# Performance work log

Hardware: AMD Instinct MI355X
Metric: run time of the kernel (lower is better)

Reference implementation:

```python
import jax, jax.numpy as jnp
import numpy as np

B, T, N, C = 8, 16, 2048, 512


def setup_inputs() -> dict:
    key = jax.random.key(0)
    k1, k2, k3, k4, k5, k6 = jax.random.split(key, 6)
    return {
        "vd_s": jax.random.normal(k1, (B, T, C), dtype=jnp.float32),
        "vd_nodes": jax.random.normal(k2, (B, N, C), dtype=jnp.float32),
        # 1x1 conv weights initialized N(0, 0.01) as in the torch module
        "W1": jax.random.normal(k3, (C, C), dtype=jnp.float32) * 0.01,
        "b1": jax.random.normal(k4, (C,), dtype=jnp.float32) * 0.01,
        "W2": jax.random.normal(k5, (C, C), dtype=jnp.float32) * 0.01,
        "b2": jax.random.normal(k6, (C,), dtype=jnp.float32) * 0.01,
    }


def reference(vd_s, vd_nodes, W1, b1, W2, b2):
    # propagation_step = 1 (as in the original module)
    def per_graph(s, nodes):
        # s: [T, C] scene features, nodes: [N, C] node features
        out_scene = s.mean(axis=0)                     # [C]
        state = nodes                                  # [N, C]
        # 1x1 convs on [N, C, 1, 1] == per-node linear layers
        mat1 = state @ W1.T + b1                       # [N, C]
        mat2 = state @ W2.T + b2                       # [N, C]
        adj = mat1 @ mat2.T                            # [N, N]
        soft_adj = jax.nn.softmax(adj, axis=1)         # row-softmax (dim=1)
        new_state = soft_adj @ state + state           # message update + residual
        gp_out = new_state.mean(axis=0)                # [C]
        return jnp.concatenate([out_scene, gp_out], axis=0)  # [2C]

    return jax.vmap(per_graph)(vd_s, vd_nodes)         # [B, 2C]
```

## Files before the change

### kernel.cpp

```cpp
#include <hip/hip_runtime.h>

typedef __bf16 bf16;
typedef __bf16 bf16x8 __attribute__((ext_vector_type(8), aligned(16)));
typedef float  f32x4  __attribute__((ext_vector_type(4)));

#define B_ 8
#define T_ 16
#define N_ 2048
#define C_ 512

__device__ inline bf16x8 load8_f32(const float* p) {
    float4 a = *(const float4*)p;
    float4 b = *(const float4*)(p + 4);
    bf16x8 r;
    r[0] = (bf16)a.x; r[1] = (bf16)a.y; r[2] = (bf16)a.z; r[3] = (bf16)a.w;
    r[4] = (bf16)b.x; r[5] = (bf16)b.y; r[6] = (bf16)b.z; r[7] = (bf16)b.w;
    return r;
}

__device__ inline void gload_lds16(const bf16* g, bf16* l) {
    __builtin_amdgcn_global_load_lds(
        (const __attribute__((address_space(1))) void*)g,
        (__attribute__((address_space(3))) void*)l, 16, 0, 0);
}

__global__ __launch_bounds__(256) void k_prep(
    const float* __restrict__ vd_s, const float* __restrict__ nodes,
    const float* __restrict__ W1, const float* __restrict__ W2,
    float* __restrict__ out, bf16* __restrict__ nodes_bf,
    bf16* __restrict__ W1t, bf16* __restrict__ W2t) {
    __shared__ float sh[32 * 33];
    const int bx = blockIdx.x, tid = threadIdx.x;
    if (bx < 2048) {
        size_t i = ((size_t)bx * 256 + tid) * 16;
        *(bf16x8*)(nodes_bf + i)     = load8_f32(nodes + i);
        *(bf16x8*)(nodes_bf + i + 8) = load8_f32(nodes + i + 8);
    } else if (bx < 2064) {
        int gt = (bx - 2048) * 256 + tid;
        int b = gt >> 9, c = gt & 511;
        float s = 0.f;
#pragma unroll
        for (int t = 0; t < T_; ++t) s += vd_s[(size_t)b * T_ * C_ + t * C_ + c];
        out[b * 2 * C_ + c] = s * (1.0f / T_);
    } else {
        const float* W = (bx < 2320) ? W1 : W2;
        bf16* Wt = (bx < 2320) ? W1t : W2t;
        int idx = (bx < 2320) ? bx - 2064 : bx - 2320;
        int bxx = (idx & 15) * 32, byy = (idx >> 4) * 32;
        int tx = tid & 31, ty = tid >> 5;
#pragma unroll
        for (int r = 0; r < 32; r += 8)
            sh[(ty + r) * 33 + tx] = W[(size_t)(byy + ty + r) * C_ + bxx + tx];
        __syncthreads();
#pragma unroll
        for (int r = 0; r < 32; r += 8)
            Wt[(size_t)(bxx + ty + r) * C_ + byy + tx] = (bf16)sh[tx * 33 + ty + r];
    }
}

__global__ void k_q(const float* __restrict__ b1, const bf16* __restrict__ W2t,
                    float* __restrict__ q) {
    int wid = threadIdx.x >> 6, lane = threadIdx.x & 63;
    int c = blockIdx.x * 4 + wid;
    bf16x8 v8 = *(const bf16x8*)(W2t + (size_t)c * C_ + lane * 8);
    float s = 0.f;
#pragma unroll
    for (int i = 0; i < 8; ++i) s += (float)v8[i] * b1[lane * 8 + i];
#pragma unroll
    for (int m = 32; m; m >>= 1) s += __shfl_xor(s, m);
    if (lane == 0) q[c] = s;
}

__global__ __launch_bounds__(256) void gemm_nt(
    const bf16* __restrict__ A, size_t strideA,
    const bf16* __restrict__ Bm, size_t strideB,
    const float* __restrict__ bias,
    bf16* __restrict__ C, size_t strideC,
    int N, int K) {
    __shared__ __attribute__((aligned(16))) bf16 lA[128 * 64];
    __shared__ __attribute__((aligned(16))) bf16 lB[128 * 64];
    const int tid = threadIdx.x;
    const int lane = tid & 63, w = tid >> 6;
    const int wm = w >> 1, wn = w & 1;
    const int z = blockIdx.z;
    const int bm = blockIdx.x * 128, bn = blockIdx.y * 128;
    const bf16* Ab = A + (size_t)z * strideA;
    const bf16* Bb = Bm + (size_t)z * strideB;

    f32x4 acc[4][4];
#pragma unroll
    for (int i = 0; i < 4; ++i)
#pragma unroll
        for (int j = 0; j < 4; ++j) acc[i][j] = f32x4{0.f, 0.f, 0.f, 0.f};

    const int nkt = K >> 6;
    for (int kt = 0; kt < nkt; ++kt) {
#pragma unroll
        for (int c = 0; c < 4; ++c) {
            int ca = c * 256 + tid;
            int row = ca >> 3;
            int qd = (ca & 7) ^ (row & 7);
            gload_lds16(Ab + (size_t)(bm + row) * K + kt * 64 + qd * 8,
                        lA + c * 2048 + w * 512);
            gload_lds16(Bb + (size_t)(bn + row) * K + kt * 64 + qd * 8,
                        lB + c * 2048 + w * 512);
        }
        __syncthreads();

        bf16x8 af[2][4], bfr[2][4];
#pragma unroll
        for (int ks = 0; ks < 2; ++ks) {
            int y = ks * 4 + (lane >> 4);
#pragma unroll
            for (int i = 0; i < 4; ++i) {
                int ra = wm * 64 + i * 16 + (lane & 15);
                int rb = wn * 64 + i * 16 + (lane & 15);
                af[ks][i]  = *(const bf16x8*)&lA[ra * 64 + ((y ^ (ra & 7)) * 8)];
                bfr[ks][i] = *(const bf16x8*)&lB[rb * 64 + ((y ^ (rb & 7)) * 8)];
            }
        }
#pragma unroll
        for (int ks = 0; ks < 2; ++ks)
#pragma unroll
            for (int i = 0; i < 4; ++i)
#pragma unroll
                for (int j = 0; j < 4; ++j)
                    acc[i][j] = __builtin_amdgcn_mfma_f32_16x16x32_bf16(
                        af[ks][i], bfr[ks][j], acc[i][j], 0, 0, 0);
        __syncthreads();
    }

    bf16* Cb = C + (size_t)z * strideC;
#pragma unroll
    for (int i = 0; i < 4; ++i) {
#pragma unroll
        for (int j = 0; j < 4; ++j) {
            int col = bn + wn * 64 + j * 16 + (lane & 15);
            float bv = bias ? bias[col] : 0.f;
#pragma unroll
            for (int r = 0; r < 4; ++r) {
                int row = bm + wm * 64 + i * 16 + (lane >> 4) * 4 + r;
                Cb[(size_t)row * N + col] = (bf16)(acc[i][j][r] + bv);
            }
        }
    }
}

__global__ __launch_bounds__(512, 2) void gemm256p(
    const bf16* __restrict__ A, const bf16* __restrict__ Bm,
    bf16* __restrict__ P) {
    __shared__ __attribute__((aligned(16))) bf16 ls[2][2][16384];
    const int tid = threadIdx.x;
    const int lane = tid & 63, w = tid >> 6;
    const int wm = w >> 2, wn = w & 3;
    const int id = blockIdx.x;
    const int sw = (id & 7) * 64 + (id >> 3);
    const int z = sw >> 6, tt = sw & 63;
    const int bm = (tt >> 3) * 256, bn = (tt & 7) * 256;
    const bf16* Ab = A + (size_t)z * N_ * C_;
    const bf16* Bb = Bm + (size_t)z * N_ * C_;

    f32x4 acc[8][4];
#pragma unroll
    for (int i = 0; i < 8; ++i)
#pragma unroll
        for (int j = 0; j < 4; ++j) acc[i][j] = f32x4{0.f, 0.f, 0.f, 0.f};

#define STAGE_H(MATP, BASE, h, kt_, buf_, abi)                                    \
    {                                                                             \
        _Pragma("unroll")                                                         \
        for (int sl = 0; sl < 2; ++sl) {                                          \
            int cc = sl * 512 + tid;                                              \
            int row = (h) * 128 + (cc >> 3);                                      \
            int qd = (cc & 7) ^ (row & 7);                                        \
            gload_lds16(MATP + (size_t)((BASE) + row) * C_ + (kt_) * 64 + qd * 8, \
                        &ls[buf_][abi][((h) * 1024 + sl * 512 + w * 64) * 8]);    \
        }                                                                         \
    }
#define STAGE_T(kt_, buf_)                                                        \
    {                                                                             \
        STAGE_H(Ab, bm, 0, kt_, buf_, 0); STAGE_H(Ab, bm, 1, kt_, buf_, 0);       \
        STAGE_H(Bb, bn, 0, kt_, buf_, 1); STAGE_H(Bb, bn, 1, kt_, buf_, 1);       \
    }

    STAGE_T(0, 0);
    STAGE_T(1, 1);
    asm volatile("s_waitcnt vmcnt(8)" ::: "memory");
    __builtin_amdgcn_s_barrier();
    asm volatile("" ::: "memory");

#pragma unroll
    for (int j = 0; j < 8; ++j) {
        const int cur = j & 1;
        const bf16* lA = &ls[cur][0][0];
        const bf16* lB = &ls[cur][1][0];

        bf16x8 af[8][2], bfv[4][2];
#pragma unroll
        for (int i = 0; i < 8; ++i) {
            int ra = wm * 128 + i * 16 + (lane & 15);
#pragma unroll
            for (int ks = 0; ks < 2; ++ks) {
                int y = ks * 4 + (lane >> 4);
                af[i][ks] = *(const bf16x8*)&lA[ra * 64 + ((y ^ (ra & 7)) * 8)];
            }
        }
#pragma unroll
        for (int jj = 0; jj < 4; ++jj) {
            int rb = wn * 64 + jj * 16 + (lane & 15);
#pragma unroll
            for (int ks = 0; ks < 2; ++ks) {
                int y = ks * 4 + (lane >> 4);
                bfv[jj][ks] = *(const bf16x8*)&lB[rb * 64 + ((y ^ (rb & 7)) * 8)];
            }
        }
        __builtin_amdgcn_s_setprio(1);
#pragma unroll
        for (int ks = 0; ks < 2; ++ks)
#pragma unroll
            for (int i = 0; i < 8; ++i)
#pragma unroll
                for (int jj = 0; jj < 4; ++jj)
                    acc[i][jj] = __builtin_amdgcn_mfma_f32_16x16x32_bf16(
                        af[i][ks], bfv[jj][ks], acc[i][jj], 0, 0, 0);
        __builtin_amdgcn_s_setprio(0);

        asm volatile("" ::: "memory");
        __builtin_amdgcn_s_barrier();
        asm volatile("" ::: "memory");

        if (j + 2 < 8) STAGE_T(j + 2, cur);
        if (j < 7) {
            if (j < 6) asm volatile("s_waitcnt vmcnt(8)" ::: "memory");
            else       asm volatile("s_waitcnt vmcnt(0)" ::: "memory");
            __builtin_amdgcn_s_barrier();
            asm volatile("" ::: "memory");
        }
    }

    bf16* Pb = P + (size_t)z * N_ * N_;
#pragma unroll
    for (int fi = 0; fi < 8; ++fi) {
#pragma unroll
        for (int fj = 0; fj < 4; ++fj) {
            int roff = (fi >> 2) * 64 + (fi & 3) * 16;
            int coff = (fj >> 1) * 32 + (fj & 1) * 16;
            int col = bn + wn * 64 + coff + (lane & 15);
#pragma unroll
            for (int r = 0; r < 4; ++r) {
                int row = bm + wm * 128 + roff + (lane >> 4) * 4 + r;
                float v = __expf(fminf(acc[fi][fj][r], 30.f));
                Pb[(size_t)row * N_ + col] = (bf16)v;
            }
        }
    }
#undef STAGE_H
#undef STAGE_T
}

__global__ __launch_bounds__(256) void k_w2(const bf16* __restrict__ P,
                                            float* __restrict__ wpart) {
    __shared__ float rp[16 * 256];
    __shared__ float ri[16];
    const int tid = threadIdx.x;
    const int s = blockIdx.x, b = blockIdx.y;
    const bf16* Pb = P + (size_t)b * N_ * N_ + (size_t)s * 16 * N_;
    const int j0 = tid * 8;
    bf16x8 v[16];
#pragma unroll
    for (int r = 0; r < 16; ++r) {
        v[r] = *(const bf16x8*)&Pb[(size_t)r * N_ + j0];
        float t = 0.f;
#pragma unroll
        for (int e = 0; e < 8; ++e) t += (float)v[r][e];
        rp[r * 256 + tid] = t;
    }
    __syncthreads();
    {
        int row = tid >> 4, seg = tid & 15;
        float t = 0.f;
#pragma unroll
        for (int k = 0; k < 16; ++k) t += rp[row * 256 + seg + 16 * k];
#pragma unroll
        for (int m = 8; m; m >>= 1) t += __shfl_xor(t, m);
        if (seg == 0) ri[row] = 1.0f / t;
    }
    __syncthreads();
    float acc8[8] = {0.f, 0.f, 0.f, 0.f, 0.f, 0.f, 0.f, 0.f};
#pragma unroll
    for (int r = 0; r < 16; ++r) {
        float rr = ri[r];
#pragma unroll
        for (int e = 0; e < 8; ++e) acc8[e] += rr * (float)v[r][e];
    }
    float* wp = wpart + ((size_t)b * 128 + s) * (size_t)N_;
#pragma unroll
    for (int e = 0; e < 8; ++e) wp[j0 + e] = acc8[e];
}

__global__ __launch_bounds__(256) void k_gp(const bf16* __restrict__ nodes_bf,
                                            const float* __restrict__ wpart,
                                            float* __restrict__ gppart) {
    __shared__ float wred[4][64];
    __shared__ float wsh[64];
    __shared__ float gred[4][512];
    const int tid = threadIdx.x;
    const int slab = blockIdx.x, b = blockIdx.y;
    const int jj = tid & 63, sg = tid >> 6;
    float wacc = 0.f;
    for (int s = sg; s < 128; s += 4)
        wacc += wpart[((size_t)b * 128 + s) * N_ + slab * 64 + jj];
    wred[sg][jj] = wacc;
    __syncthreads();
    if (tid < 64)
        wsh[tid] = wred[0][tid] + wred[1][tid] + wred[2][tid] + wred[3][tid] + 1.0f;
    __syncthreads();
    const int j0 = slab * 64;
    const int cc = (tid & 63) * 8, jr = tid >> 6;
    const bf16* nb = nodes_bf + (size_t)b * N_ * C_;
    float acc8[8] = {0.f, 0.f, 0.f, 0.f, 0.f, 0.f, 0.f, 0.f};
    for (int j = jr; j < 64; j += 4) {
        float wj = wsh[j];
        bf16x8 nv = *(const bf16x8*)&nb[(size_t)(j0 + j) * C_ + cc];
#pragma unroll
        for (int e = 0; e < 8; ++e) acc8[e] += wj * (float)nv[e];
    }
#pragma unroll
    for (int e = 0; e < 8; ++e) gred[jr][cc + e] = acc8[e];
    __syncthreads();
    if (tid < 64) {
#pragma unroll
        for (int e = 0; e < 8; ++e) {
            int c = tid * 8 + e;
            gppart[((size_t)slab * 8 + b) * C_ + c] =
                gred[0][c] + gred[1][c] + gred[2][c] + gred[3][c];
        }
    }
}

__global__ void k_fin(const float* __restrict__ gppart, float* __restrict__ out) {
    int gt = blockIdx.x * 256 + threadIdx.x;
    int b = gt >> 9, c = gt & 511;
    float s = 0.f;
#pragma unroll
    for (int k = 0; k < 32; ++k) s += gppart[((size_t)k * 8 + b) * C_ + c];
    out[b * 2 * C_ + C_ + c] = s * (1.0f / N_);
}

extern "C" void kernel_launch(void* const* d_in, const int* in_sizes, int n_in,
                              void* d_out, int out_size, void* d_ws, size_t ws_size,
                              hipStream_t stream) {
    const float* vd_s  = (const float*)d_in[0];
    const float* nodes = (const float*)d_in[1];
    const float* W1    = (const float*)d_in[2];
    const float* b1    = (const float*)d_in[3];
    const float* W2    = (const float*)d_in[4];
    float* out = (float*)d_out;

    char* ws = (char*)d_ws;
    bf16*  nodes_bf = (bf16*)(ws);
    bf16*  H2       = (bf16*)(ws + ((size_t)16 << 20));
    float* wpart    = (float*)(ws + ((size_t)16 << 20));
    bf16*  P        = (bf16*)(ws + ((size_t)32 << 20));
    bf16*  W1t      = (bf16*)(ws + ((size_t)96 << 20));
    bf16*  W2t      = (bf16*)(ws + ((size_t)96 << 20) + (512u << 10));
    bf16*  Gt       = (bf16*)(ws + ((size_t)96 << 20) + (1024u << 10));
    char*  fbase    = ws + ((size_t)96 << 20) + (1536u << 10);
    float* q        = (float*)(fbase);
    float* gppart   = (float*)(fbase + 4096);

    k_prep<<<2576, 256, 0, stream>>>(vd_s, nodes, W1, W2,
                                     out, nodes_bf, W1t, W2t);
    k_q<<<128, 256, 0, stream>>>(b1, W2t, q);

    gemm_nt<<<dim3(4, 4, 1), 256, 0, stream>>>(
        W2t, 0, W1t, 0, nullptr, Gt, 0, C_, C_);
    gemm_nt<<<dim3(16, 4, 8), 256, 0, stream>>>(
        nodes_bf, (size_t)N_ * C_, Gt, 0, q,
        H2, (size_t)N_ * C_, C_, C_);
    gemm256p<<<512, 512, 0, stream>>>(H2, nodes_bf, P);

    k_w2<<<dim3(128, 8), 256, 0, stream>>>(P, wpart);
    k_gp<<<dim3(32, 8), 256, 0, stream>>>(nodes_bf, wpart, gppart);
    k_fin<<<16, 256, 0, stream>>>(gppart, out);
}
```

Measured before the change: 130.2 us.

## Compute attention logits GEMM in FP8 with scaled H2 and fp8 node copy

The large N×N logits GEMM now takes FP8 (e4m3) operands instead of bf16. The H2 projection is written as FP8 scaled by 16, k_prep writes an extra FP8 copy of the node features, and the exp epilogue undoes the scale. This halves the operand bytes staged through LDS, halves the global loads per tile, and uses the higher-rate FP8 MFMA. In exchange the logits lose precision before the exponential, which can hurt softmax accuracy.

After: 114.9 us. -11.8%, faster.

```diff
diff --git a/kernel.cpp b/kernel.cpp
--- a/kernel.cpp
+++ b/kernel.cpp
@@ -18,23 +18,47 @@
     return r;
 }
 
-__device__ inline void gload_lds16(const bf16* g, bf16* l) {
+__device__ inline void gload_lds16(const void* g, void* l) {
     __builtin_amdgcn_global_load_lds(
         (const __attribute__((address_space(1))) void*)g,
         (__attribute__((address_space(3))) void*)l, 16, 0, 0);
+}
+
+__device__ inline unsigned char f32_to_fp8(float v) {
+    int p = __builtin_amdgcn_cvt_pk_fp8_f32(v, 0.f, 0, false);
+    return (unsigned char)(p & 0xff);
 }
 
 __global__ __launch_bounds__(256) void k_prep(
     const float* __restrict__ vd_s, const float* __restrict__ nodes,
     const float* __restrict__ W1, const float* __restrict__ W2,
     float* __restrict__ out, bf16* __restrict__ nodes_bf,
+    unsigned char* __restrict__ nodes_f8,
     bf16* __restrict__ W1t, bf16* __restrict__ W2t) {
     __shared__ float sh[32 * 33];
     const int bx = blockIdx.x, tid = threadIdx.x;
     if (bx < 2048) {
         size_t i = ((size_t)bx * 256 + tid) * 16;
-        *(bf16x8*)(nodes_bf + i)     = load8_f32(nodes + i);
-        *(bf16x8*)(nodes_bf + i + 8) = load8_f32(nodes + i + 8);
+        float v[16];
+        *(float4*)&v[0]  = *(const float4*)(nodes + i);
+        *(float4*)&v[4]  = *(const float4*)(nodes + i + 4);
+        *(float4*)&v[8]  = *(const float4*)(nodes + i + 8);
+        *(float4*)&v[12] = *(const float4*)(nodes + i + 12);
+        bf16x8 b0, b1;
+#pragma unroll
+        for (int e = 0; e < 8; ++e) { b0[e] = (bf16)v[e]; b1[e] = (bf16)v[8 + e]; }
+        *(bf16x8*)(nodes_bf + i)     = b0;
+        *(bf16x8*)(nodes_bf + i + 8) = b1;
+        uint4 u;
+        unsigned int wds[4];
+#pragma unroll
+        for (int k = 0; k < 4; ++k) {
+            int p = __builtin_amdgcn_cvt_pk_fp8_f32(v[k * 4 + 0], v[k * 4 + 1], 0, false);
+            p = __builtin_amdgcn_cvt_pk_fp8_f32(v[k * 4 + 2], v[k * 4 + 3], p, true);
+            wds[k] = (unsigned int)p;
+        }
+        u.x = wds[0]; u.y = wds[1]; u.z = wds[2]; u.w = wds[3];
+        *(uint4*)(nodes_f8 + i) = u;
     } else if (bx < 2064) {
         int gt = (bx - 2048) * 256 + tid;
         int b = gt >> 9, c = gt & 511;
@@ -71,11 +95,12 @@
     if (lane == 0) q[c] = s;
 }
 
+template <int OM>
 __global__ __launch_bounds__(256) void gemm_nt(
     const bf16* __restrict__ A, size_t strideA,
     const bf16* __restrict__ Bm, size_t strideB,
     const float* __restrict__ bias,
-    bf16* __restrict__ C, size_t strideC,
+    void* __restrict__ Cv, size_t strideC,
     int N, int K) {
     __shared__ __attribute__((aligned(16))) bf16 lA[128 * 64];
     __shared__ __attribute__((aligned(16))) bf16 lB[128 * 64];
@@ -130,7 +155,6 @@
         __syncthreads();
     }
 
-    bf16* Cb = C + (size_t)z * strideC;
 #pragma unroll
     for (int i = 0; i < 4; ++i) {
 #pragma unroll
@@ -140,25 +164,32 @@
 #pragma unroll
             for (int r = 0; r < 4; ++r) {
                 int row = bm + wm * 64 + i * 16 + (lane >> 4) * 4 + r;
-                Cb[(size_t)row * N + col] = (bf16)(acc[i][j][r] + bv);
+                float v = acc[i][j][r] + bv;
+                if constexpr (OM == 0) {
+                    ((bf16*)Cv)[(size_t)z * strideC + (size_t)row * N + col] = (bf16)v;
+                } else {
+                    ((unsigned char*)Cv)[(size_t)z * strideC + (size_t)row * N + col] =
+                        f32_to_fp8(v * 16.0f);
+                }
             }
         }
     }
 }
 
 __global__ __launch_bounds__(512, 2) void gemm256p(
-    const bf16* __restrict__ A, const bf16* __restrict__ Bm,
+    const unsigned char* __restrict__ A, const unsigned char* __restrict__ Bm,
     bf16* __restrict__ P) {
-    __shared__ __attribute__((aligned(16))) bf16 ls[2][2][16384];
+    __shared__ __attribute__((aligned(16))) unsigned char ls[2][2][16384];
     const int tid = threadIdx.x;
     const int lane = tid & 63, w = tid >> 6;
     const int wm = w >> 2, wn = w & 3;
+    const int qh = lane >> 5, ql = (lane >> 4) & 1;
     const int id = blockIdx.x;
     const int sw = (id & 7) * 64 + (id >> 3);
     const int z = sw >> 6, tt = sw & 63;
     const int bm = (tt >> 3) * 256, bn = (tt & 7) * 256;
-    const bf16* Ab = A + (size_t)z * N_ * C_;
-    const bf16* Bb = Bm + (size_t)z * N_ * C_;
+    const unsigned char* Ab = A + (size_t)z * N_ * C_;
+    const unsigned char* Bb = Bm + (size_t)z * N_ * C_;
 
     f32x4 acc[8][4];
 #pragma unroll
@@ -166,53 +197,48 @@
 #pragma unroll
         for (int j = 0; j < 4; ++j) acc[i][j] = f32x4{0.f, 0.f, 0.f, 0.f};
 
-#define STAGE_H(MATP, BASE, h, kt_, buf_, abi)                                    \
+#define STAGE_T(kt_, buf_)                                                        \
     {                                                                             \
         _Pragma("unroll")                                                         \
-        for (int sl = 0; sl < 2; ++sl) {                                          \
-            int cc = sl * 512 + tid;                                              \
-            int row = (h) * 128 + (cc >> 3);                                      \
-            int qd = (cc & 7) ^ (row & 7);                                        \
-            gload_lds16(MATP + (size_t)((BASE) + row) * C_ + (kt_) * 64 + qd * 8, \
-                        &ls[buf_][abi][((h) * 1024 + sl * 512 + w * 64) * 8]);    \
+        for (int l = 0; l < 2; ++l) {                                             \
+            int ca = l * 512 + tid;                                               \
+            int row = ca >> 2;                                                    \
+            int qd = (ca & 3) ^ ((row >> 1) & 3);                                 \
+            gload_lds16(Ab + (size_t)(bm + row) * 512 + (kt_) * 64 + qd * 16,     \
+                        &ls[buf_][0][(l * 512 + w * 64) * 16]);                   \
+            gload_lds16(Bb + (size_t)(bn + row) * 512 + (kt_) * 64 + qd * 16,     \
+                        &ls[buf_][1][(l * 512 + w * 64) * 16]);                   \
         }                                                                         \
-    }
-#define STAGE_T(kt_, buf_)                                                        \
-    {                                                                             \
-        STAGE_H(Ab, bm, 0, kt_, buf_, 0); STAGE_H(Ab, bm, 1, kt_, buf_, 0);       \
-        STAGE_H(Bb, bn, 0, kt_, buf_, 1); STAGE_H(Bb, bn, 1, kt_, buf_, 1);       \
     }
 
     STAGE_T(0, 0);
     STAGE_T(1, 1);
-    asm volatile("s_waitcnt vmcnt(8)" ::: "memory");
+    asm volatile("s_waitcnt vmcnt(4)" ::: "memory");
     __builtin_amdgcn_s_barrier();
     asm volatile("" ::: "memory");
 
 #pragma unroll
     for (int j = 0; j < 8; ++j) {
         const int cur = j & 1;
-        const bf16* lA = &ls[cur][0][0];
-        const bf16* lB = &ls[cur][1][0];
-
-        bf16x8 af[8][2], bfv[4][2];
+        const unsigned char* lA = &ls[cur][0][0];
+        const unsigned char* lB = &ls[cur][1][0];
+
+        long af[8][2], bfv[4][2];
 #pragma unroll
         for (int i = 0; i < 8; ++i) {
             int ra = wm * 128 + i * 16 + (lane & 15);
-#pragma unroll
-            for (int ks = 0; ks < 2; ++ks) {
-                int y = ks * 4 + (lane >> 4);
-                af[i][ks] = *(const bf16x8*)&lA[ra * 64 + ((y ^ (ra & 7)) * 8)];
-            }
+            int rr = (ra >> 1) & 3;
+#pragma unroll
+            for (int ks = 0; ks < 2; ++ks)
+                af[i][ks] = *(const long*)&lA[ra * 64 + (((ks * 2 + qh) ^ rr) * 16) + ql * 8];
         }
 #pragma unroll
         for (int jj = 0; jj < 4; ++jj) {
             int rb = wn * 64 + jj * 16 + (lane & 15);
-#pragma unroll
-            for (int ks = 0; ks < 2; ++ks) {
-                int y = ks * 4 + (lane >> 4);
-                bfv[jj][ks] = *(const bf16x8*)&lB[rb * 64 + ((y ^ (rb & 7)) * 8)];
-            }
+            int rr = (rb >> 1) & 3;
+#pragma unroll
+            for (int ks = 0; ks < 2; ++ks)
+                bfv[jj][ks] = *(const long*)&lB[rb * 64 + (((ks * 2 + qh) ^ rr) * 16) + ql * 8];
         }
         __builtin_amdgcn_s_setprio(1);
 #pragma unroll
@@ -221,7 +247,7 @@
             for (int i = 0; i < 8; ++i)
 #pragma unroll
                 for (int jj = 0; jj < 4; ++jj)
-                    acc[i][jj] = __builtin_amdgcn_mfma_f32_16x16x32_bf16(
+                    acc[i][jj] = __builtin_amdgcn_mfma_f32_16x16x32_fp8_fp8(
                         af[i][ks], bfv[jj][ks], acc[i][jj], 0, 0, 0);
         __builtin_amdgcn_s_setprio(0);
 
@@ -231,7 +257,7 @@
 
         if (j + 2 < 8) STAGE_T(j + 2, cur);
         if (j < 7) {
-            if (j < 6) asm volatile("s_waitcnt vmcnt(8)" ::: "memory");
+            if (j < 6) asm volatile("s_waitcnt vmcnt(4)" ::: "memory");
             else       asm volatile("s_waitcnt vmcnt(0)" ::: "memory");
             __builtin_amdgcn_s_barrier();
             asm volatile("" ::: "memory");
@@ -249,12 +275,11 @@
 #pragma unroll
             for (int r = 0; r < 4; ++r) {
                 int row = bm + wm * 128 + roff + (lane >> 4) * 4 + r;
-                float v = __expf(fminf(acc[fi][fj][r], 30.f));
+                float v = __expf(fminf(acc[fi][fj][r] * 0.0625f, 30.f));
                 Pb[(size_t)row * N_ + col] = (bf16)v;
             }
         }
     }
-#undef STAGE_H
 #undef STAGE_T
 }
 
@@ -358,27 +383,28 @@
     float* out = (float*)d_out;
 
     char* ws = (char*)d_ws;
-    bf16*  nodes_bf = (bf16*)(ws);
-    bf16*  H2       = (bf16*)(ws + ((size_t)16 << 20));
-    float* wpart    = (float*)(ws + ((size_t)16 << 20));
-    bf16*  P        = (bf16*)(ws + ((size_t)32 << 20));
-    bf16*  W1t      = (bf16*)(ws + ((size_t)96 << 20));
-    bf16*  W2t      = (bf16*)(ws + ((size_t)96 << 20) + (512u << 10));
-    bf16*  Gt       = (bf16*)(ws + ((size_t)96 << 20) + (1024u << 10));
-    char*  fbase    = ws + ((size_t)96 << 20) + (1536u << 10);
-    float* q        = (float*)(fbase);
-    float* gppart   = (float*)(fbase + 4096);
+    bf16*          nodes_bf = (bf16*)(ws);
+    unsigned char* H2f8     = (unsigned char*)(ws + ((size_t)16 << 20));
+    float*         wpart    = (float*)(ws + ((size_t)16 << 20));
+    unsigned char* nodes_f8 = (unsigned char*)(ws + ((size_t)24 << 20));
+    bf16*          P        = (bf16*)(ws + ((size_t)32 << 20));
+    bf16*          W1t      = (bf16*)(ws + ((size_t)96 << 20));
+    bf16*          W2t      = (bf16*)(ws + ((size_t)96 << 20) + (512u << 10));
+    bf16*          Gt       = (bf16*)(ws + ((size_t)96 << 20) + (1024u << 10));
+    char*          fbase    = ws + ((size_t)96 << 20) + (1536u << 10);
+    float*         q        = (float*)(fbase);
+    float*         gppart   = (float*)(fbase + 4096);
 
     k_prep<<<2576, 256, 0, stream>>>(vd_s, nodes, W1, W2,
-                                     out, nodes_bf, W1t, W2t);
+                                     out, nodes_bf, nodes_f8, W1t, W2t);
     k_q<<<128, 256, 0, stream>>>(b1, W2t, q);
 
-    gemm_nt<<<dim3(4, 4, 1), 256, 0, stream>>>(
+    gemm_nt<0><<<dim3(4, 4, 1), 256, 0, stream>>>(
         W2t, 0, W1t, 0, nullptr, Gt, 0, C_, C_);
-    gemm_nt<<<dim3(16, 4, 8), 256, 0, stream>>>(
+    gemm_nt<1><<<dim3(16, 4, 8), 256, 0, stream>>>(
         nodes_bf, (size_t)N_ * C_, Gt, 0, q,
-        H2, (size_t)N_ * C_, C_, C_);
-    gemm256p<<<512, 512, 0, stream>>>(H2, nodes_bf, P);
+        H2f8, (size_t)N_ * C_, C_, C_);
+    gemm256p<<<512, 512, 0, stream>>>(H2f8, nodes_f8, P);
 
     k_w2<<<dim3(128, 8), 256, 0, stream>>>(P, wpart);
     k_gp<<<dim3(32, 8), 256, 0, stream>>>(nodes_bf, wpart, gppart);
```
